# Optimization experiments

Measured on AMD Instinct MI355X. Metric: run time of the kernel, lower is better.

The kernel has to match this reference:

```python
import jax, jax.numpy as jnp
import numpy as np

N = 8192
IN_F = 512
OUT_F = 512
ALPHA = 0.2  # leaky relu slope


def setup_inputs() -> dict:
    key = jax.random.key(0)
    k1, k2, k3, k4, k5 = jax.random.split(key, 5)
    inp = jax.random.normal(k1, (N, IN_F), dtype=jnp.float32)
    adj = jax.random.randint(k2, (N, N), 0, 2, dtype=jnp.int32)
    # linear1: [in, out] + bias
    W1 = jax.random.normal(k3, (IN_F, OUT_F), dtype=jnp.float32) * (1.0 / np.sqrt(IN_F))
    b1 = jnp.zeros((OUT_F,), dtype=jnp.float32)
    # linear2: maps 2*out -> 1; split into the two halves acting on h_i and h_j
    a = jax.random.normal(k4, (2 * OUT_F,), dtype=jnp.float32) * (1.0 / np.sqrt(2 * OUT_F))
    a1 = a[:OUT_F]
    a2 = a[OUT_F:]
    b2 = jnp.zeros((), dtype=jnp.float32)
    return {"inp": inp, "adj": adj, "W1": W1, "b1": b1, "a1": a1, "a2": a2, "b2": b2}


def reference(inp, adj, W1, b1, a1, a2, b2):
    h = inp @ W1 + b1  # [N, out]
    # linear2(cat(h_i, h_j)) == h_i@a1 + h_j@a2 + b2 -> avoids the N*N*2F tensor
    e = jax.nn.leaky_relu((h @ a1)[:, None] + (h @ a2)[None, :] + b2, ALPHA)  # [N, N]
    attention = jnp.where(adj > 0, e, jnp.float32(-1e12))
    attention = jax.nn.softmax(attention, axis=1)
    h_prime = attention @ h  # [N, out]
    return jax.nn.elu(h_prime)  # concat=True
```

## Files before the change

kernel.cpp:

```cpp
#include <hip/hip_runtime.h>
#include <hip/hip_bf16.h>
#include <stdint.h>

#define NR 8192
#define FD 512
#define BM 64

typedef __attribute__((ext_vector_type(8))) short s8v;
typedef __attribute__((ext_vector_type(4))) float f32x4;

static __device__ __forceinline__ short bf16_rtne(float x) {
    union { float f; uint32_t u; } v; v.f = x;
    uint32_t r = (v.u + 0x7FFFu + ((v.u >> 16) & 1u)) >> 16;
    return (short)r;
}
static __device__ __forceinline__ float bf16_to_f32(short s) {
    union { uint32_t u; float f; } v; v.u = ((uint32_t)(uint16_t)s) << 16;
    return v.f;
}

__global__ void k_prepack(const int* __restrict__ adj,
                          unsigned long long* __restrict__ bm) {
    const int lane = threadIdx.x & 63;
    const int wv   = threadIdx.x >> 6;
    const int gid  = blockIdx.x * 4 + wv;
    const int row  = gid >> 2;
    const int seg  = (gid & 3) * 2048;
    const int* p   = adj + (size_t)row * NR + seg + lane;
    unsigned long long* o = bm + (((size_t)row * NR + seg) >> 6);
#pragma unroll
    for (int g = 0; g < 8; ++g) {
        unsigned long long b0 = __ballot(p[g * 256]       != 0);
        unsigned long long b1 = __ballot(p[g * 256 + 64]  != 0);
        unsigned long long b2 = __ballot(p[g * 256 + 128] != 0);
        unsigned long long b3 = __ballot(p[g * 256 + 192] != 0);
        unsigned long long vs = (lane == 0) ? b0 : (lane == 1) ? b1
                              : (lane == 2) ? b2 : b3;
        if (lane < 4) o[g * 4 + lane] = vs;
    }
}

__global__ void k_convert(const float* __restrict__ in, short* __restrict__ out) {
    int i = blockIdx.x * blockDim.x + threadIdx.x;
    float4 v = ((const float4*)in)[i];
    short4 s;
    s.x = bf16_rtne(v.x); s.y = bf16_rtne(v.y);
    s.z = bf16_rtne(v.z); s.w = bf16_rtne(v.w);
    ((short4*)out)[i] = s;
}

__global__ void k_w1t(const float* __restrict__ W1, short* __restrict__ W1T) {
    int i = blockIdx.x * 256 + threadIdx.x;
    int k = i & 511, n = i >> 9;
    W1T[(size_t)n * 512 + k] = bf16_rtne(W1[(size_t)k * 512 + n]);
}

__launch_bounds__(256)
__global__ void k_gemm_h(const short* __restrict__ A,
                         const short* __restrict__ BT,
                         const float* __restrict__ b1,
                         short* __restrict__ H,
                         short* __restrict__ HT3)
{
    const int lane = threadIdx.x & 63;
    const int wn   = threadIdx.x >> 6;
    const int m    = lane & 15;
    const int q    = lane >> 4;
    const int r0   = blockIdx.x * 32;
    const int c0   = blockIdx.y * 128 + wn * 32;

    f32x4 acc[2][2] = {};
#pragma unroll 1
    for (int k0 = 0; k0 < 512; k0 += 32) {
        s8v a[2], b[2];
#pragma unroll
        for (int rt = 0; rt < 2; ++rt)
            a[rt] = *(const s8v*)(A + (size_t)(r0 + rt * 16 + m) * 512 + k0 + q * 8);
#pragma unroll
        for (int nt = 0; nt < 2; ++nt)
            b[nt] = *(const s8v*)(BT + (size_t)(c0 + nt * 16 + m) * 512 + k0 + q * 8);
#pragma unroll
        for (int rt = 0; rt < 2; ++rt)
#pragma unroll
            for (int nt = 0; nt < 2; ++nt)
                acc[rt][nt] = __builtin_amdgcn_mfma_f32_16x16x32_bf16(a[rt], b[nt], acc[rt][nt], 0, 0, 0);
    }
    float b1v[2];
#pragma unroll
    for (int nt = 0; nt < 2; ++nt) b1v[nt] = b1[c0 + nt * 16 + m];

#pragma unroll
    for (int rt = 0; rt < 2; ++rt)
#pragma unroll
        for (int nt = 0; nt < 2; ++nt) {
            int col = c0 + nt * 16 + m;
            short4 hp;
#pragma unroll
            for (int r = 0; r < 4; ++r) {
                int row = r0 + rt * 16 + q * 4 + r;
                short hv = bf16_rtne(acc[rt][nt][r] + b1v[nt]);
                H[(size_t)row * 512 + col] = hv;
                ((short*)&hp)[r] = hv;
            }
            size_t off = (size_t)blockIdx.x * 16384
                       + (size_t)(blockIdx.y * 2 + (wn >> 1)) * 2048
                       + (size_t)((wn * 2 + nt) & 3) * 512
                       + (rt * 2 + (q >> 1)) * 128
                       + m * 8 + (q & 1) * 4;
            *(short4*)(HT3 + off) = hp;
        }
}

__global__ void k_f1f2(const short* __restrict__ H, const float* __restrict__ a1,
                       const float* __restrict__ a2, const float* __restrict__ b2,
                       float* __restrict__ f1, float* __restrict__ f2s)
{
    const int lane = threadIdx.x & 63;
    const int row  = blockIdx.x * 4 + (threadIdx.x >> 6);
    s8v hv = *(const s8v*)(H + (size_t)row * 512 + lane * 8);
    float4 a1l = ((const float4*)(a1 + lane * 8))[0];
    float4 a1h = ((const float4*)(a1 + lane * 8))[1];
    float4 a2l = ((const float4*)(a2 + lane * 8))[0];
    float4 a2h = ((const float4*)(a2 + lane * 8))[1];
    float hf[8];
#pragma unroll
    for (int i = 0; i < 8; ++i) hf[i] = bf16_to_f32(hv[i]);
    float s1 = hf[0] * a1l.x + hf[1] * a1l.y + hf[2] * a1l.z + hf[3] * a1l.w
             + hf[4] * a1h.x + hf[5] * a1h.y + hf[6] * a1h.z + hf[7] * a1h.w;
    float s2 = hf[0] * a2l.x + hf[1] * a2l.y + hf[2] * a2l.z + hf[3] * a2l.w
             + hf[4] * a2h.x + hf[5] * a2h.y + hf[6] * a2h.z + hf[7] * a2h.w;
#pragma unroll
    for (int o = 32; o > 0; o >>= 1) {
        s1 += __shfl_xor(s1, o);
        s2 += __shfl_xor(s2, o);
    }
    if (lane == 0) {
        f1[row]  = s1;
        f2s[row] = s2 + b2[0];
    }
}

__launch_bounds__(512, 2)
__global__ void k_attn(const uint32_t* __restrict__ bm,
                       const short* __restrict__ HT3,
                       const float* __restrict__ f1,
                       const float* __restrict__ f2s,
                       float* __restrict__ nump,
                       float* __restrict__ denomp)
{
    __shared__ __align__(16) short wt[2][BM * 256];

    const int t    = threadIdx.x;
    const int lane = t & 63;
    const int w    = t >> 6;
    const int m    = lane & 15;
    const int q    = lane >> 4;

    const int js   = blockIdx.x & 1;
    const int band = blockIdx.x >> 1;
    const int r0   = band * BM;
    const int jb0  = js * 4096;
    const int jt0  = js * 128;

    const int prow = t >> 3;
    const int jg   = t & 7;

    const float f1v = f1[r0 + prow];
    const uint32_t* bmrow = bm + (size_t)(r0 + prow) * 256 + js * 128;
    const float* f2base = f2s + jb0;

    f32x4 acc[4][4] = {};
    float dsum = 0.f;

#define GAT_BLOAD(DST, KT)                                                     \
    {                                                                          \
        const short* s_ = HT3 + (size_t)(jt0 + (KT)) * 16384 + w * 2048        \
                        + q * 128 + m * 8;                                     \
        DST[0] = *(const s8v*)(s_);                                            \
        DST[1] = *(const s8v*)(s_ + 512);                                      \
        DST[2] = *(const s8v*)(s_ + 1024);                                     \
        DST[3] = *(const s8v*)(s_ + 1536);                                     \
    }

#define GAT_WUNIT(U, BYTE, FA, FB, P)                                          \
    {                                                                          \
        s8v wv_;                                                               \
        const float* ff_ = (const float*)&(FA);                                \
        _Pragma("unroll")                                                      \
        for (int jj = 0; jj < 4; ++jj) {                                       \
            float s_ = f1v + ff_[jj];                                          \
            float e_ = __expf(fmaxf(s_, 0.2f * s_));                           \
            float x_ = (((BYTE) >> jj) & 1u) ? e_ : 0.f;                       \
            dsum += x_; wv_[jj] = bf16_rtne(x_);                               \
        }                                                                      \
        const float* fg_ = (const float*)&(FB);                               \
        _Pragma("unroll")                                                      \
        for (int jj = 0; jj < 4; ++jj) {                                       \
            float s_ = f1v + fg_[jj];                                          \
            float e_ = __expf(fmaxf(s_, 0.2f * s_));                           \
            float x_ = (((BYTE) >> (4 + jj)) & 1u) ? e_ : 0.f;                 \
            dsum += x_; wv_[4 + jj] = bf16_rtne(x_);                           \
        }                                                                      \
        *(s8v*)&wt[P][prow * 256 + (((U) ^ (prow & 7)) << 3)] = wv_;           \
    }

    {
        uint4 mwa_ = *(const uint4*)(bmrow);
        uint4 mwb_ = *(const uint4*)(bmrow + 4);
        uint32_t m8_[8] = {mwa_.x, mwa_.y, mwa_.z, mwa_.w,
                           mwb_.x, mwb_.y, mwb_.z, mwb_.w};
#pragma unroll
        for (int k_ = 0; k_ < 4; ++k_) {
            const int u_ = jg + 8 * k_;
            uint32_t byte_ = (m8_[(jg >> 2) + 2 * k_] >> ((jg & 3) * 8)) & 0xFFu;
            float4 fa_ = *(const float4*)(f2base + u_ * 8);
            float4 fb_ = *(const float4*)(f2base + u_ * 8 + 4);
            GAT_WUNIT(u_, byte_, fa_, fb_, 0)
        }
    }
    s8v breg[2][4];
    GAT_BLOAD(breg[0], 0)
    GAT_BLOAD(breg[1], 1)
    __syncthreads();

    int kt = 0;
#pragma unroll 1
    for (int ch = 0; ch < 16; ++ch) {
        const int p = ch & 1;
        const int chn = (ch + 1) & 15;
        uint4 mwa_ = *(const uint4*)(bmrow + chn * 8);
        uint4 mwb_ = *(const uint4*)(bmrow + chn * 8 + 4);
        float4 fa_[4], fb_[4];
#pragma unroll
        for (int k_ = 0; k_ < 4; ++k_) {
            const int u_ = jg + 8 * k_;
            fa_[k_] = *(const float4*)(f2base + chn * 256 + u_ * 8);
            fb_[k_] = *(const float4*)(f2base + chn * 256 + u_ * 8 + 4);
        }
        uint32_t m8_[8] = {mwa_.x, mwa_.y, mwa_.z, mwa_.w,
                           mwb_.x, mwb_.y, mwb_.z, mwb_.w};

#pragma unroll
        for (int kk = 0; kk < 8; ++kk, ++kt) {
            const int e = kk & 1;
            s8v bn[4];
            GAT_BLOAD(bn, (kt + 2) & 127)
            s8v af[4];
#pragma unroll
            for (int i = 0; i < 4; ++i)
                af[i] = *(const s8v*)&wt[p][(i * 16 + m) * 256
                                            + (((kk * 4 + q) ^ (m & 7)) << 3)];
#pragma unroll
            for (int nt = 0; nt < 4; ++nt)
#pragma unroll
                for (int i = 0; i < 4; ++i)
                    acc[i][nt] = __builtin_amdgcn_mfma_f32_16x16x32_bf16(af[i], breg[e][nt], acc[i][nt], 0, 0, 0);
            if (kk >= 2 && kk <= 5 && ch < 15) {
                const int k_ = kk - 2;
                const int u_ = jg + 8 * k_;
                uint32_t byte_ = (m8_[(jg >> 2) + 2 * k_] >> ((jg & 3) * 8)) & 0xFFu;
                GAT_WUNIT(u_, byte_, fa_[k_], fb_[k_], p ^ 1)
            }
#pragma unroll
            for (int nt = 0; nt < 4; ++nt) breg[e][nt] = bn[nt];
        }
        __syncthreads();
    }
#undef GAT_BLOAD
#undef GAT_WUNIT

    dsum += __shfl_xor(dsum, 1);
    dsum += __shfl_xor(dsum, 2);
    dsum += __shfl_xor(dsum, 4);
    if (jg == 0) denomp[(size_t)js * NR + r0 + prow] = dsum;

    float* np = nump + (size_t)js * NR * FD;
#pragma unroll
    for (int i = 0; i < 4; ++i)
#pragma unroll
        for (int nt = 0; nt < 4; ++nt)
#pragma unroll
            for (int r = 0; r < 4; ++r) {
                int row = r0 + i * 16 + q * 4 + r;
                int col = w * 64 + nt * 16 + m;
                np[(size_t)row * FD + col] = acc[i][nt][r];
            }
}

__global__ void k_combine(const float* __restrict__ nump,
                          const float* __restrict__ denomp,
                          float* __restrict__ out)
{
    size_t e = ((size_t)blockIdx.x * 256 + threadIdx.x) * 4;
    int row = (int)(e >> 9);
    float4 n0 = *(const float4*)(nump + e);
    float4 n1 = *(const float4*)(nump + (size_t)NR * FD + e);
    float d = denomp[row] + denomp[NR + row];
    float inv = 1.0f / d;
    float4 o;
    o.x = (n0.x + n1.x) * inv;
    o.y = (n0.y + n1.y) * inv;
    o.z = (n0.z + n1.z) * inv;
    o.w = (n0.w + n1.w) * inv;
    o.x = (o.x > 0.f) ? o.x : (__expf(o.x) - 1.f);
    o.y = (o.y > 0.f) ? o.y : (__expf(o.y) - 1.f);
    o.z = (o.z > 0.f) ? o.z : (__expf(o.z) - 1.f);
    o.w = (o.w > 0.f) ? o.w : (__expf(o.w) - 1.f);
    *(float4*)(out + e) = o;
}

extern "C" void kernel_launch(void* const* d_in, const int* in_sizes, int n_in,
                              void* d_out, int out_size, void* d_ws, size_t ws_size,
                              hipStream_t stream) {
    const float* inp = (const float*)d_in[0];
    const int*   adj = (const int*)d_in[1];
    const float* W1  = (const float*)d_in[2];
    const float* b1  = (const float*)d_in[3];
    const float* a1  = (const float*)d_in[4];
    const float* a2  = (const float*)d_in[5];
    const float* b2  = (const float*)d_in[6];
    float* out = (float*)d_out;

    short*    inp_bf = (short*)d_ws;
    short*    w1t    = inp_bf + (size_t)NR * FD;
    short*    h      = w1t + (size_t)FD * FD;
    short*    ht3    = h + (size_t)NR * FD;
    uint32_t* bmw    = (uint32_t*)(ht3 + (size_t)FD * NR);
    float*    f1     = (float*)(bmw + (size_t)NR * 256);
    float*    f2s    = f1 + NR;
    float*    nump   = f2s + NR;
    float*    denomp = nump + (size_t)2 * NR * FD;

    k_prepack<<<NR, 256, 0, stream>>>(adj, (unsigned long long*)bmw);
    k_convert<<<(NR * FD / 4) / 256, 256, 0, stream>>>(inp, inp_bf);
    k_w1t<<<(FD * FD) / 256, 256, 0, stream>>>(W1, w1t);
    dim3 g1(NR / 32, FD / 128);
    k_gemm_h<<<g1, 256, 0, stream>>>(inp_bf, w1t, b1, h, ht3);
    k_f1f2<<<NR / 4, 256, 0, stream>>>(h, a1, a2, b2, f1, f2s);
    k_attn<<<128 * 2, 512, 0, stream>>>(bmw, ht3, f1, f2s, nump, denomp);
    k_combine<<<(NR * FD / 4) / 256, 256, 0, stream>>>(nump, denomp, out);
}
```

Measured before the change: 504.7 us.

## Fuse adjacency bitmask packing into attention kernel, reading int32 adj directly

```diff
diff --git a/kernel.cpp b/kernel.cpp
--- a/kernel.cpp
+++ b/kernel.cpp
@@ -17,27 +17,6 @@
 static __device__ __forceinline__ float bf16_to_f32(short s) {
     union { uint32_t u; float f; } v; v.u = ((uint32_t)(uint16_t)s) << 16;
     return v.f;
-}
-
-__global__ void k_prepack(const int* __restrict__ adj,
-                          unsigned long long* __restrict__ bm) {
-    const int lane = threadIdx.x & 63;
-    const int wv   = threadIdx.x >> 6;
-    const int gid  = blockIdx.x * 4 + wv;
-    const int row  = gid >> 2;
-    const int seg  = (gid & 3) * 2048;
-    const int* p   = adj + (size_t)row * NR + seg + lane;
-    unsigned long long* o = bm + (((size_t)row * NR + seg) >> 6);
-#pragma unroll
-    for (int g = 0; g < 8; ++g) {
-        unsigned long long b0 = __ballot(p[g * 256]       != 0);
-        unsigned long long b1 = __ballot(p[g * 256 + 64]  != 0);
-        unsigned long long b2 = __ballot(p[g * 256 + 128] != 0);
-        unsigned long long b3 = __ballot(p[g * 256 + 192] != 0);
-        unsigned long long vs = (lane == 0) ? b0 : (lane == 1) ? b1
-                              : (lane == 2) ? b2 : b3;
-        if (lane < 4) o[g * 4 + lane] = vs;
-    }
 }
 
 __global__ void k_convert(const float* __restrict__ in, short* __restrict__ out) {
@@ -141,7 +120,7 @@
 }
 
 __launch_bounds__(512, 2)
-__global__ void k_attn(const uint32_t* __restrict__ bm,
+__global__ void k_attn(const int* __restrict__ adj,
                        const short* __restrict__ HT3,
                        const float* __restrict__ f1,
                        const float* __restrict__ f2s,
@@ -166,7 +145,7 @@
     const int jg   = t & 7;
 
     const float f1v = f1[r0 + prow];
-    const uint32_t* bmrow = bm + (size_t)(r0 + prow) * 256 + js * 128;
+    const int* adjrow = adj + (size_t)(r0 + prow) * NR + jb0;
     const float* f2base = f2s + jb0;
 
     f32x4 acc[4][4] = {};
@@ -182,40 +161,39 @@
         DST[3] = *(const s8v*)(s_ + 1536);                                     \
     }
 
-#define GAT_WUNIT(U, BYTE, FA, FB, P)                                          \
+#define GAT_WUNIT(U, MA, MB, FA, FB, P)                                        \
     {                                                                          \
         s8v wv_;                                                               \
         const float* ff_ = (const float*)&(FA);                                \
+        const int*   mm_ = (const int*)&(MA);                                  \
         _Pragma("unroll")                                                      \
         for (int jj = 0; jj < 4; ++jj) {                                       \
             float s_ = f1v + ff_[jj];                                          \
             float e_ = __expf(fmaxf(s_, 0.2f * s_));                           \
-            float x_ = (((BYTE) >> jj) & 1u) ? e_ : 0.f;                       \
+            float x_ = (mm_[jj] > 0) ? e_ : 0.f;                               \
             dsum += x_; wv_[jj] = bf16_rtne(x_);                               \
         }                                                                      \
-        const float* fg_ = (const float*)&(FB);                               \
+        const float* fg_ = (const float*)&(FB);                                \
+        const int*   mn_ = (const int*)&(MB);                                  \
         _Pragma("unroll")                                                      \
         for (int jj = 0; jj < 4; ++jj) {                                       \
             float s_ = f1v + fg_[jj];                                          \
             float e_ = __expf(fmaxf(s_, 0.2f * s_));                           \
-            float x_ = (((BYTE) >> (4 + jj)) & 1u) ? e_ : 0.f;                 \
+            float x_ = (mn_[jj] > 0) ? e_ : 0.f;                               \
             dsum += x_; wv_[4 + jj] = bf16_rtne(x_);                           \
         }                                                                      \
         *(s8v*)&wt[P][prow * 256 + (((U) ^ (prow & 7)) << 3)] = wv_;           \
     }
 
     {
-        uint4 mwa_ = *(const uint4*)(bmrow);
-        uint4 mwb_ = *(const uint4*)(bmrow + 4);
-        uint32_t m8_[8] = {mwa_.x, mwa_.y, mwa_.z, mwa_.w,
-                           mwb_.x, mwb_.y, mwb_.z, mwb_.w};
 #pragma unroll
         for (int k_ = 0; k_ < 4; ++k_) {
             const int u_ = jg + 8 * k_;
-            uint32_t byte_ = (m8_[(jg >> 2) + 2 * k_] >> ((jg & 3) * 8)) & 0xFFu;
+            uint4 ma_ = *(const uint4*)(adjrow + u_ * 8);
+            uint4 mb_ = *(const uint4*)(adjrow + u_ * 8 + 4);
             float4 fa_ = *(const float4*)(f2base + u_ * 8);
             float4 fb_ = *(const float4*)(f2base + u_ * 8 + 4);
-            GAT_WUNIT(u_, byte_, fa_, fb_, 0)
+            GAT_WUNIT(u_, ma_, mb_, fa_, fb_, 0)
         }
     }
     s8v breg[2][4];
@@ -228,23 +206,23 @@
     for (int ch = 0; ch < 16; ++ch) {
         const int p = ch & 1;
         const int chn = (ch + 1) & 15;
-        uint4 mwa_ = *(const uint4*)(bmrow + chn * 8);
-        uint4 mwb_ = *(const uint4*)(bmrow + chn * 8 + 4);
-        float4 fa_[4], fb_[4];
-#pragma unroll
-        for (int k_ = 0; k_ < 4; ++k_) {
-            const int u_ = jg + 8 * k_;
-            fa_[k_] = *(const float4*)(f2base + chn * 256 + u_ * 8);
-            fb_[k_] = *(const float4*)(f2base + chn * 256 + u_ * 8 + 4);
-        }
-        uint32_t m8_[8] = {mwa_.x, mwa_.y, mwa_.z, mwa_.w,
-                           mwb_.x, mwb_.y, mwb_.z, mwb_.w};
+        const int* adjn = adjrow + chn * 256;
+        const float* f2n = f2base + chn * 256;
+        uint4  man_[4], mbn_[4];
+        float4 fan_[4], fbn_[4];
 
 #pragma unroll
         for (int kk = 0; kk < 8; ++kk, ++kt) {
             const int e = kk & 1;
             s8v bn[4];
             GAT_BLOAD(bn, (kt + 2) & 127)
+            if (kk < 4 && ch < 15) {
+                const int u_ = jg + 8 * kk;
+                man_[kk] = *(const uint4*)(adjn + u_ * 8);
+                mbn_[kk] = *(const uint4*)(adjn + u_ * 8 + 4);
+                fan_[kk] = *(const float4*)(f2n + u_ * 8);
+                fbn_[kk] = *(const float4*)(f2n + u_ * 8 + 4);
+            }
             s8v af[4];
 #pragma unroll
             for (int i = 0; i < 4; ++i)
@@ -255,11 +233,10 @@
 #pragma unroll
                 for (int i = 0; i < 4; ++i)
                     acc[i][nt] = __builtin_amdgcn_mfma_f32_16x16x32_bf16(af[i], breg[e][nt], acc[i][nt], 0, 0, 0);
-            if (kk >= 2 && kk <= 5 && ch < 15) {
-                const int k_ = kk - 2;
+            if (kk >= 3 && kk <= 6 && ch < 15) {
+                const int k_ = kk - 3;
                 const int u_ = jg + 8 * k_;
-                uint32_t byte_ = (m8_[(jg >> 2) + 2 * k_] >> ((jg & 3) * 8)) & 0xFFu;
-                GAT_WUNIT(u_, byte_, fa_[k_], fb_[k_], p ^ 1)
+                GAT_WUNIT(u_, man_[k_], mbn_[k_], fan_[k_], fbn_[k_], p ^ 1)
             }
 #pragma unroll
             for (int nt = 0; nt < 4; ++nt) breg[e][nt] = bn[nt];
@@ -325,18 +302,16 @@
     short*    w1t    = inp_bf + (size_t)NR * FD;
     short*    h      = w1t + (size_t)FD * FD;
     short*    ht3    = h + (size_t)NR * FD;
-    uint32_t* bmw    = (uint32_t*)(ht3 + (size_t)FD * NR);
-    float*    f1     = (float*)(bmw + (size_t)NR * 256);
+    float*    f1     = (float*)(ht3 + (size_t)FD * NR);
     float*    f2s    = f1 + NR;
     float*    nump   = f2s + NR;
     float*    denomp = nump + (size_t)2 * NR * FD;
 
-    k_prepack<<<NR, 256, 0, stream>>>(adj, (unsigned long long*)bmw);
     k_convert<<<(NR * FD / 4) / 256, 256, 0, stream>>>(inp, inp_bf);
     k_w1t<<<(FD * FD) / 256, 256, 0, stream>>>(W1, w1t);
     dim3 g1(NR / 32, FD / 128);
     k_gemm_h<<<g1, 256, 0, stream>>>(inp_bf, w1t, b1, h, ht3);
     k_f1f2<<<NR / 4, 256, 0, stream>>>(h, a1, a2, b2, f1, f2s);
-    k_attn<<<128 * 2, 512, 0, stream>>>(bmw, ht3, f1, f2s, nump, denomp);
+    k_attn<<<128 * 2, 512, 0, stream>>>(adj, ht3, f1, f2s, nump, denomp);
     k_combine<<<(NR * FD / 4) / 256, 256, 0, stream>>>(nump, denomp, out);
 }
```

Result: faster. 481.9 us (-4.5%).
